# Performance work log

Measured on AMD Instinct MI355X. Metric: run time of the kernel, lower is better.

Reference implementation:

```python
import jax, jax.numpy as jnp
import numpy as np

N = 100000
E = 3200000
IN_DIM = 128
HID = 64
BN_EPS = 1e-5


def _gcn_conv(x, W, b, src, dst, dinv):
    h = x @ W                                      # [N, out]
    coeff = (dinv[src] * dinv[dst])[:, None]       # [E, 1]
    msg = h[src] * coeff                           # gather over edges
    agg = jax.ops.segment_sum(msg, dst, num_segments=N)
    agg = agg + h * (dinv * dinv)[:, None]         # self-loop term
    return agg + b


def setup_inputs() -> dict:
    key = jax.random.key(0)
    ks = jax.random.split(key, 12)
    x = jax.random.normal(ks[0], (N, IN_DIM), dtype=jnp.float32)
    edge_index = jax.random.randint(ks[1], (2, E), 0, N, dtype=jnp.int64)
    s1 = 1.0 / np.sqrt(IN_DIM)
    s2 = 1.0 / np.sqrt(HID)
    W1 = jax.random.uniform(ks[2], (IN_DIM, HID), jnp.float32, -s1, s1)
    b1 = jnp.zeros((HID,), jnp.float32)
    W2 = jax.random.uniform(ks[3], (HID, HID), jnp.float32, -s2, s2)
    b2 = jnp.zeros((HID,), jnp.float32)
    W3 = jax.random.uniform(ks[4], (HID, 1), jnp.float32, -s2, s2)
    b3 = jnp.zeros((1,), jnp.float32)
    g1 = jnp.ones((HID,), jnp.float32)
    beta1 = jnp.zeros((HID,), jnp.float32)
    m1 = 0.1 * jax.random.normal(ks[5], (HID,), jnp.float32)
    v1 = jax.random.uniform(ks[6], (HID,), jnp.float32) + 0.5
    g2 = jnp.ones((HID,), jnp.float32)
    beta2 = jnp.zeros((HID,), jnp.float32)
    m2 = 0.1 * jax.random.normal(ks[7], (HID,), jnp.float32)
    v2 = jax.random.uniform(ks[8], (HID,), jnp.float32) + 0.5
    return {"x": x, "edge_index": edge_index,
            "W1": W1, "b1": b1, "W2": W2, "b2": b2, "W3": W3, "b3": b3,
            "g1": g1, "beta1": beta1, "m1": m1, "v1": v1,
            "g2": g2, "beta2": beta2, "m2": m2, "v2": v2}


def reference(x, edge_index, W1, b1, W2, b2, W3, b3,
              g1, beta1, m1, v1, g2, beta2, m2, v2):
    src, dst = edge_index[0], edge_index[1]
    # degree with self-loops (computed on destination index, PyG convention)
    deg = jax.ops.segment_sum(jnp.ones((E,), jnp.float32), dst, num_segments=N) + 1.0
    dinv = jax.lax.rsqrt(deg)

    def bn(h, g, beta, m, v):
        return (h - m) * jax.lax.rsqrt(v + BN_EPS) * g + beta

    h = _gcn_conv(x, W1, b1, src, dst, dinv)
    h = jax.nn.relu(bn(h, g1, beta1, m1, v1))  # dropout is a no-op in eval
    h = _gcn_conv(h, W2, b2, src, dst, dinv)
    h = jax.nn.relu(bn(h, g2, beta2, m2, v2))
    h = _gcn_conv(h, W3, b3, src, dst, dinv)
    return jax.nn.sigmoid(h)  # [N, 1]
```

## Files before the change

kernel.cpp:

```cpp
#include <hip/hip_runtime.h>
#include <math.h>

#define N_NODES 100000
#define E_EDGES 3200000
#define IN_DIM_ 128
#define HID_ 64
#define BN_EPS_ 1e-5f

#define PB 250
#define CHUNK 12800
#define NBUCK 391
#define BMAX 9600
#define SUB (N_NODES + 1)

typedef __attribute__((ext_vector_type(8))) short short8;
typedef __attribute__((ext_vector_type(4))) float f32x4;

__device__ inline ushort f2bf(float f) {
    union { float f; unsigned u; } c; c.f = f;
    unsigned r = c.u + 0x7fff + ((c.u >> 16) & 1);
    return (ushort)(r >> 16);
}
__device__ inline float bf_lo(unsigned p) { union { unsigned u; float f; } c; c.u = p << 16; return c.f; }
__device__ inline float bf_hi(unsigned p) { union { unsigned u; float f; } c; c.u = p & 0xffff0000u; return c.f; }

__global__ __launch_bounds__(512) void passA1_hist(const int* __restrict__ ei,
                                                   int* __restrict__ histPB) {
    __shared__ int hist[NBUCK];
    int t = threadIdx.x, b = blockIdx.x;
    for (int k = t; k < NBUCK; k += 512) hist[k] = 0;
    __syncthreads();
    int e0 = b * CHUNK, e1 = e0 + CHUNK;
    for (int e = e0 + t; e < e1; e += 512) {
        int d = ei[E_EDGES + e];
        atomicAdd(&hist[d >> 8], 1);
    }
    __syncthreads();
    for (int k = t; k < NBUCK; k += 512) histPB[k * PB + b] = hist[k];
}

__global__ __launch_bounds__(256) void scan_rows(int* __restrict__ histPB,
                                                 int* __restrict__ bucket_tot) {
    __shared__ int wsum[4];
    int k = blockIdx.x, t = threadIdx.x, lane = t & 63, wv = t >> 6;
    int v = (t < PB) ? histPB[k * PB + t] : 0;
    int s = v;
#pragma unroll
    for (int off = 1; off < 64; off <<= 1) {
        int u = __shfl_up(s, off, 64);
        if (lane >= off) s += u;
    }
    if (lane == 63) wsum[wv] = s;
    __syncthreads();
    int wbase = 0;
    for (int w = 0; w < wv; w++) wbase += wsum[w];
    if (t < PB) histPB[k * PB + t] = wbase + s - v;
    if (t == 255) bucket_tot[k] = wbase + s;
}

__global__ __launch_bounds__(512) void scan_totals(const int* __restrict__ bucket_tot,
                                                   int* __restrict__ bucket_base,
                                                   float* __restrict__ hs3) {
    __shared__ int wsum[8];
    int t = threadIdx.x, lane = t & 63, wv = t >> 6;
    int v = (t < NBUCK) ? bucket_tot[t] : 0;
    int s = v;
#pragma unroll
    for (int off = 1; off < 64; off <<= 1) {
        int u = __shfl_up(s, off, 64);
        if (lane >= off) s += u;
    }
    if (lane == 63) wsum[wv] = s;
    __syncthreads();
    int wbase = 0;
    for (int w = 0; w < wv; w++) wbase += wsum[w];
    if (t < NBUCK) bucket_base[t] = wbase + s - v;
    if (t == 0) {
        bucket_base[NBUCK] = E_EDGES;
        hs3[N_NODES] = 0.f;
    }
}

__global__ __launch_bounds__(512) void passA2_sorted(const int* __restrict__ ei,
                                                     const int* __restrict__ histPB,
                                                     const int* __restrict__ bucket_base,
                                                     int* __restrict__ ebuf) {
    __shared__ int sorted[CHUNK];
    __shared__ ushort bid[CHUNK];
    __shared__ int cur[NBUCK];
    __shared__ int lbase[NBUCK];
    int t = threadIdx.x, b = blockIdx.x;
    for (int k = t; k < NBUCK; k += 512) cur[k] = 0;
    __syncthreads();
    int e0 = b * CHUNK;
    for (int e = e0 + t; e < e0 + CHUNK; e += 512)
        atomicAdd(&cur[ei[E_EDGES + e] >> 8], 1);
    __syncthreads();
    if (t < 64) {
        int run = 0;
        for (int c0 = 0; c0 < NBUCK; c0 += 64) {
            int idx = c0 + t;
            int v = (idx < NBUCK) ? cur[idx] : 0;
            int s = v;
#pragma unroll
            for (int off = 1; off < 64; off <<= 1) {
                int u = __shfl_up(s, off, 64);
                if (t >= off) s += u;
            }
            if (idx < NBUCK) lbase[idx] = run + s - v;
            run += __shfl(s, 63, 64);
        }
    }
    __syncthreads();
    for (int k = t; k < NBUCK; k += 512) cur[k] = lbase[k];
    __syncthreads();
    for (int e = e0 + t; e < e0 + CHUNK; e += 512) {
        int s = ei[e];
        int d = ei[E_EDGES + e];
        int k = d >> 8;
        int pos = atomicAdd(&cur[k], 1);
        sorted[pos] = s | ((d & 255) << 17);
        bid[pos] = (ushort)k;
    }
    __syncthreads();
    for (int j = t; j < CHUNK; j += 512) {
        int k = bid[j];
        int dest = bucket_base[k] + histPB[k * PB + b] + (j - lbase[k]);
        ebuf[dest] = sorted[j];
    }
}

__global__ __launch_bounds__(256) void bucket_deg(const int* __restrict__ ebuf,
                                                  const int* __restrict__ bucket_base,
                                                  int* __restrict__ deg,
                                                  float* __restrict__ dinv,
                                                  int* __restrict__ bucket_ptot) {
    __shared__ int hist[256];
    __shared__ int wsum[4];
    int b = blockIdx.x, t = threadIdx.x, lane = t & 63, wv = t >> 6;
    int base = bucket_base[b], end = bucket_base[b + 1];
    hist[t] = 0;
    __syncthreads();
    for (int k = base + t; k < end; k += 256)
        atomicAdd(&hist[ebuf[k] >> 17], 1);
    __syncthreads();
    int node = b * 256 + t;
    int d = hist[t];
    if (node < N_NODES) {
        deg[node] = d;
        dinv[node] = rsqrtf((float)d + 1.0f);
    }
    int pd = (node < N_NODES) ? ((d + 15) & ~15) : 0;
#pragma unroll
    for (int off = 1; off < 64; off <<= 1) pd += __shfl_xor(pd, off, 64);
    if (lane == 0) wsum[wv] = pd;
    __syncthreads();
    if (t == 0) bucket_ptot[b] = wsum[0] + wsum[1] + wsum[2] + wsum[3];
}

__global__ __launch_bounds__(512) void scan_ptot(const int* __restrict__ bucket_ptot,
                                                 int* __restrict__ bucket_pbase,
                                                 int* __restrict__ row_ptr) {
    __shared__ int wsum[8];
    int t = threadIdx.x, lane = t & 63, wv = t >> 6;
    int v = (t < NBUCK) ? bucket_ptot[t] : 0;
    int s = v;
#pragma unroll
    for (int off = 1; off < 64; off <<= 1) {
        int u = __shfl_up(s, off, 64);
        if (lane >= off) s += u;
    }
    if (lane == 63) wsum[wv] = s;
    __syncthreads();
    int wbase = 0;
    for (int w = 0; w < wv; w++) wbase += wsum[w];
    if (t < NBUCK) bucket_pbase[t] = wbase + s - v;
    if (t == NBUCK - 1) row_ptr[N_NODES] = wbase + s;
}

__global__ __launch_bounds__(256) void passB_sorted(const int* __restrict__ ebuf,
                                                    const int* __restrict__ bucket_base,
                                                    const int* __restrict__ bucket_pbase,
                                                    const int* __restrict__ deg,
                                                    int* __restrict__ row_ptr,
                                                    int* __restrict__ csr_src) {
    __shared__ int sorted[BMAX];
    __shared__ int ucur[256];
    __shared__ int ubeg[256];
    __shared__ int pbeg[256];
    __shared__ int wsA[4], wsB[4];
    int b = blockIdx.x, t = threadIdx.x, lane = t & 63, wv = t >> 6;
    int base = bucket_base[b], end = bucket_base[b + 1];
    int pbase = bucket_pbase[b];
    int node = b * 256 + t;
    int d = (node < N_NODES) ? deg[node] : 0;
    int pd = (d + 15) & ~15;
    if (node >= N_NODES) pd = 0;
    int sa = d, sb = pd;
#pragma unroll
    for (int off = 1; off < 64; off <<= 1) {
        int ua = __shfl_up(sa, off, 64);
        int ub = __shfl_up(sb, off, 64);
        if (lane >= off) { sa += ua; sb += ub; }
    }
    if (lane == 63) { wsA[wv] = sa; wsB[wv] = sb; }
    __syncthreads();
    int wa = 0, wb = 0;
    for (int w = 0; w < wv; w++) { wa += wsA[w]; wb += wsB[w]; }
    int uex = wa + sa - d, pex = wb + sb - pd;
    ubeg[t] = uex; pbeg[t] = pex; ucur[t] = uex;
    if (node < N_NODES) row_ptr[node] = pbase + pex;
    __syncthreads();
    for (int k = base + t; k < end; k += 256) {
        int pv = ebuf[k];
        int pos = atomicAdd(&ucur[pv >> 17], 1);
        if (pos < BMAX) sorted[pos] = pv;
    }
    __syncthreads();
    for (int r = wv; r < 256; r += 4) {
        int nd = b * 256 + r;
        int d2 = (nd < N_NODES) ? deg[nd] : 0;
        int pd2 = (nd < N_NODES) ? ((d2 + 15) & ~15) : 0;
        int ub = ubeg[r], pb = pbeg[r];
        for (int c = lane; c < pd2; c += 64)
            csr_src[pbase + pb + c] = (c < d2) ? (sorted[ub + c] & 0x1FFFF) : N_NODES;
    }
}

template<bool LAST, int P>
__global__ __launch_bounds__(256) void gather_pass(const int* __restrict__ row_ptr,
                                                   const int* __restrict__ csr_src,
                                                   const ushort* __restrict__ hs,
                                                   const float* __restrict__ dinv,
                                                   const float* __restrict__ b,
                                                   const float* __restrict__ g,
                                                   const float* __restrict__ beta,
                                                   const float* __restrict__ m,
                                                   const float* __restrict__ v,
                                                   unsigned* __restrict__ y,
                                                   const float* __restrict__ W3,
                                                   float* __restrict__ hs3, int n) {
    int i = (blockIdx.x * 256 + threadIdx.x) >> 6;
    if (i >= n) return;
    int l = threadIdx.x & 63;
    int es = l >> 2, fg = l & 3;

    const uint4* T4 = (const uint4*)((const unsigned*)hs + (long)P * SUB * 16);

    float a0 = 0.f, a1 = 0.f, a2 = 0.f, a3 = 0.f;
    float a4 = 0.f, a5 = 0.f, a6 = 0.f, a7 = 0.f;

    if (es == 0) {
        uint4 p = T4[(unsigned)i * 4 + fg];
        a0 += bf_lo(p.x); a1 += bf_hi(p.x);
        a2 += bf_lo(p.y); a3 += bf_hi(p.y);
        a4 += bf_lo(p.z); a5 += bf_hi(p.z);
        a6 += bf_lo(p.w); a7 += bf_hi(p.w);
    }

    int pbeg = row_ptr[i], pend = row_ptr[i + 1];
    const int* cs = csr_src + pbeg + es;
    int nb16 = (pend - pbeg) >> 4;
    int k = 0;
    for (; k + 2 <= nb16; k += 2) {
        int sA = cs[0];
        int sB = cs[16];
        cs += 32;
        uint4 pA = T4[(unsigned)sA * 4 + fg];
        uint4 pB = T4[(unsigned)sB * 4 + fg];
        a0 += bf_lo(pA.x) + bf_lo(pB.x); a1 += bf_hi(pA.x) + bf_hi(pB.x);
        a2 += bf_lo(pA.y) + bf_lo(pB.y); a3 += bf_hi(pA.y) + bf_hi(pB.y);
        a4 += bf_lo(pA.z) + bf_lo(pB.z); a5 += bf_hi(pA.z) + bf_hi(pB.z);
        a6 += bf_lo(pA.w) + bf_lo(pB.w); a7 += bf_hi(pA.w) + bf_hi(pB.w);
    }
    if (k < nb16) {
        int s = cs[0];
        uint4 p = T4[(unsigned)s * 4 + fg];
        a0 += bf_lo(p.x); a1 += bf_hi(p.x);
        a2 += bf_lo(p.y); a3 += bf_hi(p.y);
        a4 += bf_lo(p.z); a5 += bf_hi(p.z);
        a6 += bf_lo(p.w); a7 += bf_hi(p.w);
    }

#pragma unroll
    for (int off = 4; off < 64; off <<= 1) {
        a0 += __shfl_xor(a0, off, 64);
        a1 += __shfl_xor(a1, off, 64);
        a2 += __shfl_xor(a2, off, 64);
        a3 += __shfl_xor(a3, off, 64);
        a4 += __shfl_xor(a4, off, 64);
        a5 += __shfl_xor(a5, off, 64);
        a6 += __shfl_xor(a6, off, 64);
        a7 += __shfl_xor(a7, off, 64);
    }

    int fb = P * 8 + fg * 2;
    float4 bb0 = ((const float4*)b)[fb],    bb1 = ((const float4*)b)[fb + 1];
    float4 gg0 = ((const float4*)g)[fb],    gg1 = ((const float4*)g)[fb + 1];
    float4 be0 = ((const float4*)beta)[fb], be1 = ((const float4*)beta)[fb + 1];
    float4 mm0 = ((const float4*)m)[fb],    mm1 = ((const float4*)m)[fb + 1];
    float4 vv0 = ((const float4*)v)[fb],    vv1 = ((const float4*)v)[fb + 1];
    float di = dinv[i];
    float o0 = fmaxf((di * a0 + bb0.x - mm0.x) * (gg0.x * rsqrtf(vv0.x + BN_EPS_)) + be0.x, 0.f);
    float o1 = fmaxf((di * a1 + bb0.y - mm0.y) * (gg0.y * rsqrtf(vv0.y + BN_EPS_)) + be0.y, 0.f);
    float o2 = fmaxf((di * a2 + bb0.z - mm0.z) * (gg0.z * rsqrtf(vv0.z + BN_EPS_)) + be0.z, 0.f);
    float o3 = fmaxf((di * a3 + bb0.w - mm0.w) * (gg0.w * rsqrtf(vv0.w + BN_EPS_)) + be0.w, 0.f);
    float o4 = fmaxf((di * a4 + bb1.x - mm1.x) * (gg1.x * rsqrtf(vv1.x + BN_EPS_)) + be1.x, 0.f);
    float o5 = fmaxf((di * a5 + bb1.y - mm1.y) * (gg1.y * rsqrtf(vv1.y + BN_EPS_)) + be1.y, 0.f);
    float o6 = fmaxf((di * a6 + bb1.z - mm1.z) * (gg1.z * rsqrtf(vv1.z + BN_EPS_)) + be1.z, 0.f);
    float o7 = fmaxf((di * a7 + bb1.w - mm1.w) * (gg1.w * rsqrtf(vv1.w + BN_EPS_)) + be1.w, 0.f);

    if (LAST) {
        float4 w30 = ((const float4*)W3)[fb], w31 = ((const float4*)W3)[fb + 1];
        float p = o0 * w30.x + o1 * w30.y + o2 * w30.z + o3 * w30.w +
                  o4 * w31.x + o5 * w31.y + o6 * w31.z + o7 * w31.w;
        p += __shfl_xor(p, 1, 64);
        p += __shfl_xor(p, 2, 64);
        if (l == 0) {
            if (P == 0) hs3[i] = p;
            else        hs3[i] = (hs3[i] + p) * di;
        }
    } else {
        if (es == 0) {
            uint4 pk;
            pk.x = (unsigned)f2bf(o0) | ((unsigned)f2bf(o1) << 16);
            pk.y = (unsigned)f2bf(o2) | ((unsigned)f2bf(o3) << 16);
            pk.z = (unsigned)f2bf(o4) | ((unsigned)f2bf(o5) << 16);
            pk.w = (unsigned)f2bf(o6) | ((unsigned)f2bf(o7) << 16);
            ((uint4*)y)[(long)i * 8 + P * 4 + fg] = pk;
        }
    }
}

template<int K, bool BF16IN>
__global__ __launch_bounds__(256) void gemm_bf16(const void* __restrict__ Xv,
                                                 const float* __restrict__ W,
                                                 const float* __restrict__ dinv,
                                                 ushort* __restrict__ hs) {
    constexpr int KP = K + 8;
    __shared__ ushort A_lds[64][KP];
    __shared__ ushort Wt_lds[64][KP];
    int t = threadIdx.x;
    long row0 = (long)blockIdx.x * 64;

    for (int i = t; i < K * 16; i += 256) {
        float4 w4 = ((const float4*)W)[i];
        int k = i >> 4, n = (i & 15) * 4;
        Wt_lds[n + 0][k] = f2bf(w4.x);
        Wt_lds[n + 1][k] = f2bf(w4.y);
        Wt_lds[n + 2][k] = f2bf(w4.z);
        Wt_lds[n + 3][k] = f2bf(w4.w);
    }
    if (BF16IN) {
        constexpr int K2 = K / 2;
        const unsigned* X = (const unsigned*)Xv;
        for (int i = t; i < 64 * K2; i += 256) {
            int r = i / K2, c = i % K2;
            unsigned val = 0;
            long row = row0 + r;
            if (row < N_NODES) val = X[row * K2 + c];
            *(unsigned*)&A_lds[r][c * 2] = val;
        }
    } else {
        constexpr int K4 = K / 4;
        const float* X = (const float*)Xv;
        for (int i = t; i < 64 * K4; i += 256) {
            int r = i / K4, c = i % K4;
            float4 val = make_float4(0.f, 0.f, 0.f, 0.f);
            long row = row0 + r;
            if (row < N_NODES) val = ((const float4*)X)[row * K4 + c];
            int cb = c * 4;
            A_lds[r][cb + 0] = f2bf(val.x);
            A_lds[r][cb + 1] = f2bf(val.y);
            A_lds[r][cb + 2] = f2bf(val.z);
            A_lds[r][cb + 3] = f2bf(val.w);
        }
    }
    __syncthreads();

    int w = t >> 6, l = t & 63;
    int m = l & 15, quad = l >> 4;
    f32x4 acc[4];
#pragma unroll
    for (int c = 0; c < 4; c++) acc[c] = (f32x4){0.f, 0.f, 0.f, 0.f};

#pragma unroll
    for (int ch = 0; ch < K / 32; ch++) {
        short8 a = *(const short8*)&A_lds[16 * w + m][32 * ch + 8 * quad];
#pragma unroll
        for (int c = 0; c < 4; c++) {
            short8 b = *(const short8*)&Wt_lds[16 * c + m][32 * ch + 8 * quad];
            acc[c] = __builtin_amdgcn_mfma_f32_16x16x32_bf16(a, b, acc[c], 0, 0, 0);
        }
    }

#pragma unroll
    for (int r = 0; r < 4; r++) {
        long node = row0 + 16 * w + quad * 4 + r;
        if (node <= N_NODES) {
            float dv = (node < N_NODES) ? dinv[node] : 0.f;
#pragma unroll
            for (int c = 0; c < 4; c++)
                hs[((long)(c >> 1) * SUB + node) * 32 + (c & 1) * 16 + m] = f2bf(acc[c][r] * dv);
        }
    }
}

__global__ __launch_bounds__(256) void gather3(const int* __restrict__ row_ptr,
                                               const int* __restrict__ csr_src,
                                               const float* __restrict__ hs3,
                                               const float* __restrict__ dinv,
                                               const float* __restrict__ b3,
                                               float* __restrict__ out, int n) {
    int i = blockIdx.x * 256 + threadIdx.x;
    if (i >= n) return;
    int beg = row_ptr[i], end = row_ptr[i + 1];
    float s0 = hs3[i], s1 = 0.f, s2 = 0.f, s3 = 0.f;
    float s4 = 0.f, s5 = 0.f, s6 = 0.f, s7 = 0.f;
    for (int k = beg; k + 8 <= end; k += 8) {
        s0 += hs3[csr_src[k]];
        s1 += hs3[csr_src[k + 1]];
        s2 += hs3[csr_src[k + 2]];
        s3 += hs3[csr_src[k + 3]];
        s4 += hs3[csr_src[k + 4]];
        s5 += hs3[csr_src[k + 5]];
        s6 += hs3[csr_src[k + 6]];
        s7 += hs3[csr_src[k + 7]];
    }
    float z = dinv[i] * (((s0 + s1) + (s2 + s3)) + ((s4 + s5) + (s6 + s7))) + b3[0];
    out[i] = 1.f / (1.f + expf(-z));
}

extern "C" void kernel_launch(void* const* d_in, const int* in_sizes, int n_in,
                              void* d_out, int out_size, void* d_ws, size_t ws_size,
                              hipStream_t stream) {
    const int N = N_NODES;
    const int E = E_EDGES;

    const float* x   = (const float*)d_in[0];
    const int*   ei  = (const int*)d_in[1];
    const float* W1  = (const float*)d_in[2];
    const float* b1  = (const float*)d_in[3];
    const float* W2  = (const float*)d_in[4];
    const float* b2  = (const float*)d_in[5];
    const float* W3  = (const float*)d_in[6];
    const float* b3  = (const float*)d_in[7];
    const float* g1  = (const float*)d_in[8];
    const float* bt1 = (const float*)d_in[9];
    const float* m1  = (const float*)d_in[10];
    const float* v1  = (const float*)d_in[11];
    const float* g2  = (const float*)d_in[12];
    const float* bt2 = (const float*)d_in[13];
    const float* m2  = (const float*)d_in[14];
    const float* v2  = (const float*)d_in[15];
    float* out = (float*)d_out;

    int*    wsi          = (int*)d_ws;
    float*  dinv         = (float*)wsi;
    float*  hs3          = (float*)(wsi + (long)N);
    int*    row_ptr      = wsi + 2L * N + 16;
    int*    deg          = row_ptr + N + 16;
    int*    histPB       = deg + N + 16;
    int*    bucket_tot   = histPB + NBUCK * PB;
    int*    bucket_base  = bucket_tot + 400;
    int*    bucket_ptot  = bucket_base + 402;
    int*    bucket_pbase = bucket_ptot + 400;
    ushort* hsb          = (ushort*)(bucket_pbase + 402);
    unsigned* yb         = (unsigned*)((int*)(void*)hsb + 32L * SUB);
    int*    csr_src      = (int*)yb + 32L * N;
    int*    ebuf         = (int*)(void*)hsb;

    passA1_hist<<<PB, 512, 0, stream>>>(ei, histPB);
    scan_rows<<<NBUCK, 256, 0, stream>>>(histPB, bucket_tot);
    scan_totals<<<1, 512, 0, stream>>>(bucket_tot, bucket_base, hs3);
    passA2_sorted<<<PB, 512, 0, stream>>>(ei, histPB, bucket_base, ebuf);
    bucket_deg<<<NBUCK, 256, 0, stream>>>(ebuf, bucket_base, deg, dinv, bucket_ptot);
    scan_ptot<<<1, 512, 0, stream>>>(bucket_ptot, bucket_pbase, row_ptr);
    passB_sorted<<<NBUCK, 256, 0, stream>>>(ebuf, bucket_base, bucket_pbase,
                                            deg, row_ptr, csr_src);

    const int GG = (N + 3) / 4;

    gemm_bf16<IN_DIM_, false><<<(N + 63) / 64, 256, 0, stream>>>(x, W1, dinv, hsb);
    gather_pass<false, 0><<<GG, 256, 0, stream>>>(row_ptr, csr_src, hsb, dinv,
                                                  b1, g1, bt1, m1, v1, yb, W3, hs3, N);
    gather_pass<false, 1><<<GG, 256, 0, stream>>>(row_ptr, csr_src, hsb, dinv,
                                                  b1, g1, bt1, m1, v1, yb, W3, hs3, N);
    gemm_bf16<HID_, true><<<(N + 63) / 64, 256, 0, stream>>>(yb, W2, dinv, hsb);
    gather_pass<true, 0><<<GG, 256, 0, stream>>>(row_ptr, csr_src, hsb, dinv,
                                                 b2, g2, bt2, m2, v2, yb, W3, hs3, N);
    gather_pass<true, 1><<<GG, 256, 0, stream>>>(row_ptr, csr_src, hsb, dinv,
                                                 b2, g2, bt2, m2, v2, yb, W3, hs3, N);
    gather3<<<(N + 255) / 256, 256, 0, stream>>>(row_ptr, csr_src, hs3, dinv, b3, out, N);
}
```

Before: 489.9 us.

## Merge two half-feature gather passes into one full-width gather per layer

Replaces the two gather passes per layer, each handling 32 of the 64 features, with a single pass. Each wave now covers all 64 features using 8 lanes per edge and 8 edge slots, so csr_src is read once per layer instead of twice and two kernel launches are removed. CSR row padding drops from multiples of 16 to multiples of 8 to match the new edge stride, which cuts the number of padded dummy edges. The gather loop is unrolled to four loads per lane per iteration for more memory parallelism. In exchange, each pass touches the whole feature table, so cache locality per pass may be worse than with the two half-width tables.

```diff
diff --git a/kernel.cpp b/kernel.cpp
--- a/kernel.cpp
+++ b/kernel.cpp
@@ -150,7 +150,7 @@
         deg[node] = d;
         dinv[node] = rsqrtf((float)d + 1.0f);
     }
-    int pd = (node < N_NODES) ? ((d + 15) & ~15) : 0;
+    int pd = (node < N_NODES) ? ((d + 7) & ~7) : 0;
 #pragma unroll
     for (int off = 1; off < 64; off <<= 1) pd += __shfl_xor(pd, off, 64);
     if (lane == 0) wsum[wv] = pd;
@@ -194,7 +194,7 @@
     int pbase = bucket_pbase[b];
     int node = b * 256 + t;
     int d = (node < N_NODES) ? deg[node] : 0;
-    int pd = (d + 15) & ~15;
+    int pd = (d + 7) & ~7;
     if (node >= N_NODES) pd = 0;
     int sa = d, sb = pd;
 #pragma unroll
@@ -220,15 +220,15 @@
     for (int r = wv; r < 256; r += 4) {
         int nd = b * 256 + r;
         int d2 = (nd < N_NODES) ? deg[nd] : 0;
-        int pd2 = (nd < N_NODES) ? ((d2 + 15) & ~15) : 0;
+        int pd2 = (nd < N_NODES) ? ((d2 + 7) & ~7) : 0;
         int ub = ubeg[r], pb = pbeg[r];
         for (int c = lane; c < pd2; c += 64)
             csr_src[pbase + pb + c] = (c < d2) ? (sorted[ub + c] & 0x1FFFF) : N_NODES;
     }
 }
 
-template<bool LAST, int P>
-__global__ __launch_bounds__(256) void gather_pass(const int* __restrict__ row_ptr,
+template<bool LAST>
+__global__ __launch_bounds__(256) void gather_full(const int* __restrict__ row_ptr,
                                                    const int* __restrict__ csr_src,
                                                    const ushort* __restrict__ hs,
                                                    const float* __restrict__ dinv,
@@ -243,15 +243,15 @@
     int i = (blockIdx.x * 256 + threadIdx.x) >> 6;
     if (i >= n) return;
     int l = threadIdx.x & 63;
-    int es = l >> 2, fg = l & 3;
-
-    const uint4* T4 = (const uint4*)((const unsigned*)hs + (long)P * SUB * 16);
+    int es = l >> 3, fg = l & 7;
+
+    const uint4* Tq = (const uint4*)hs + (long)(fg >> 2) * SUB * 4 + (fg & 3);
 
     float a0 = 0.f, a1 = 0.f, a2 = 0.f, a3 = 0.f;
     float a4 = 0.f, a5 = 0.f, a6 = 0.f, a7 = 0.f;
 
     if (es == 0) {
-        uint4 p = T4[(unsigned)i * 4 + fg];
+        uint4 p = Tq[(unsigned)i * 4];
         a0 += bf_lo(p.x); a1 += bf_hi(p.x);
         a2 += bf_lo(p.y); a3 += bf_hi(p.y);
         a4 += bf_lo(p.z); a5 += bf_hi(p.z);
@@ -260,22 +260,28 @@
 
     int pbeg = row_ptr[i], pend = row_ptr[i + 1];
     const int* cs = csr_src + pbeg + es;
-    int nb16 = (pend - pbeg) >> 4;
-    int k = 0;
-    for (; k + 2 <= nb16; k += 2) {
-        int sA = cs[0];
-        int sB = cs[16];
+    int nb8 = (pend - pbeg) >> 3;
+    int full = nb8 >> 2;
+    for (int t = 0; t < full; t++) {
+        int s0 = cs[0], s1 = cs[8], s2 = cs[16], s3 = cs[24];
         cs += 32;
-        uint4 pA = T4[(unsigned)sA * 4 + fg];
-        uint4 pB = T4[(unsigned)sB * 4 + fg];
-        a0 += bf_lo(pA.x) + bf_lo(pB.x); a1 += bf_hi(pA.x) + bf_hi(pB.x);
-        a2 += bf_lo(pA.y) + bf_lo(pB.y); a3 += bf_hi(pA.y) + bf_hi(pB.y);
-        a4 += bf_lo(pA.z) + bf_lo(pB.z); a5 += bf_hi(pA.z) + bf_hi(pB.z);
-        a6 += bf_lo(pA.w) + bf_lo(pB.w); a7 += bf_hi(pA.w) + bf_hi(pB.w);
-    }
-    if (k < nb16) {
+        uint4 p0 = Tq[(unsigned)s0 * 4];
+        uint4 p1 = Tq[(unsigned)s1 * 4];
+        uint4 p2 = Tq[(unsigned)s2 * 4];
+        uint4 p3 = Tq[(unsigned)s3 * 4];
+        a0 += bf_lo(p0.x) + bf_lo(p1.x); a1 += bf_hi(p0.x) + bf_hi(p1.x);
+        a2 += bf_lo(p0.y) + bf_lo(p1.y); a3 += bf_hi(p0.y) + bf_hi(p1.y);
+        a4 += bf_lo(p0.z) + bf_lo(p1.z); a5 += bf_hi(p0.z) + bf_hi(p1.z);
+        a6 += bf_lo(p0.w) + bf_lo(p1.w); a7 += bf_hi(p0.w) + bf_hi(p1.w);
+        a0 += bf_lo(p2.x) + bf_lo(p3.x); a1 += bf_hi(p2.x) + bf_hi(p3.x);
+        a2 += bf_lo(p2.y) + bf_lo(p3.y); a3 += bf_hi(p2.y) + bf_hi(p3.y);
+        a4 += bf_lo(p2.z) + bf_lo(p3.z); a5 += bf_hi(p2.z) + bf_hi(p3.z);
+        a6 += bf_lo(p2.w) + bf_lo(p3.w); a7 += bf_hi(p2.w) + bf_hi(p3.w);
+    }
+    for (int rem = nb8 & 3; rem > 0; rem--) {
         int s = cs[0];
-        uint4 p = T4[(unsigned)s * 4 + fg];
+        cs += 8;
+        uint4 p = Tq[(unsigned)s * 4];
         a0 += bf_lo(p.x); a1 += bf_hi(p.x);
         a2 += bf_lo(p.y); a3 += bf_hi(p.y);
         a4 += bf_lo(p.z); a5 += bf_hi(p.z);
@@ -283,7 +289,7 @@
     }
 
 #pragma unroll
-    for (int off = 4; off < 64; off <<= 1) {
+    for (int off = 8; off < 64; off <<= 1) {
         a0 += __shfl_xor(a0, off, 64);
         a1 += __shfl_xor(a1, off, 64);
         a2 += __shfl_xor(a2, off, 64);
@@ -294,12 +300,11 @@
         a7 += __shfl_xor(a7, off, 64);
     }
 
-    int fb = P * 8 + fg * 2;
-    float4 bb0 = ((const float4*)b)[fb],    bb1 = ((const float4*)b)[fb + 1];
-    float4 gg0 = ((const float4*)g)[fb],    gg1 = ((const float4*)g)[fb + 1];
-    float4 be0 = ((const float4*)beta)[fb], be1 = ((const float4*)beta)[fb + 1];
-    float4 mm0 = ((const float4*)m)[fb],    mm1 = ((const float4*)m)[fb + 1];
-    float4 vv0 = ((const float4*)v)[fb],    vv1 = ((const float4*)v)[fb + 1];
+    float4 bb0 = ((const float4*)b)[fg * 2],    bb1 = ((const float4*)b)[fg * 2 + 1];
+    float4 gg0 = ((const float4*)g)[fg * 2],    gg1 = ((const float4*)g)[fg * 2 + 1];
+    float4 be0 = ((const float4*)beta)[fg * 2], be1 = ((const float4*)beta)[fg * 2 + 1];
+    float4 mm0 = ((const float4*)m)[fg * 2],    mm1 = ((const float4*)m)[fg * 2 + 1];
+    float4 vv0 = ((const float4*)v)[fg * 2],    vv1 = ((const float4*)v)[fg * 2 + 1];
     float di = dinv[i];
     float o0 = fmaxf((di * a0 + bb0.x - mm0.x) * (gg0.x * rsqrtf(vv0.x + BN_EPS_)) + be0.x, 0.f);
     float o1 = fmaxf((di * a1 + bb0.y - mm0.y) * (gg0.y * rsqrtf(vv0.y + BN_EPS_)) + be0.y, 0.f);
@@ -311,15 +316,13 @@
     float o7 = fmaxf((di * a7 + bb1.w - mm1.w) * (gg1.w * rsqrtf(vv1.w + BN_EPS_)) + be1.w, 0.f);
 
     if (LAST) {
-        float4 w30 = ((const float4*)W3)[fb], w31 = ((const float4*)W3)[fb + 1];
+        float4 w30 = ((const float4*)W3)[fg * 2], w31 = ((const float4*)W3)[fg * 2 + 1];
         float p = o0 * w30.x + o1 * w30.y + o2 * w30.z + o3 * w30.w +
                   o4 * w31.x + o5 * w31.y + o6 * w31.z + o7 * w31.w;
-        p += __shfl_xor(p, 1, 64);
-        p += __shfl_xor(p, 2, 64);
-        if (l == 0) {
-            if (P == 0) hs3[i] = p;
-            else        hs3[i] = (hs3[i] + p) * di;
-        }
+#pragma unroll
+        for (int off = 1; off < 8; off <<= 1)
+            p += __shfl_xor(p, off, 64);
+        if (l == 0) hs3[i] = p * di;
     } else {
         if (es == 0) {
             uint4 pk;
@@ -327,7 +330,7 @@
             pk.y = (unsigned)f2bf(o2) | ((unsigned)f2bf(o3) << 16);
             pk.z = (unsigned)f2bf(o4) | ((unsigned)f2bf(o5) << 16);
             pk.w = (unsigned)f2bf(o6) | ((unsigned)f2bf(o7) << 16);
-            ((uint4*)y)[(long)i * 8 + P * 4 + fg] = pk;
+            ((uint4*)y)[(long)i * 8 + fg] = pk;
         }
     }
 }
@@ -482,14 +485,10 @@
     const int GG = (N + 3) / 4;
 
     gemm_bf16<IN_DIM_, false><<<(N + 63) / 64, 256, 0, stream>>>(x, W1, dinv, hsb);
-    gather_pass<false, 0><<<GG, 256, 0, stream>>>(row_ptr, csr_src, hsb, dinv,
-                                                  b1, g1, bt1, m1, v1, yb, W3, hs3, N);
-    gather_pass<false, 1><<<GG, 256, 0, stream>>>(row_ptr, csr_src, hsb, dinv,
-                                                  b1, g1, bt1, m1, v1, yb, W3, hs3, N);
+    gather_full<false><<<GG, 256, 0, stream>>>(row_ptr, csr_src, hsb, dinv,
+                                               b1, g1, bt1, m1, v1, yb, W3, hs3, N);
     gemm_bf16<HID_, true><<<(N + 63) / 64, 256, 0, stream>>>(yb, W2, dinv, hsb);
-    gather_pass<true, 0><<<GG, 256, 0, stream>>>(row_ptr, csr_src, hsb, dinv,
-                                                 b2, g2, bt2, m2, v2, yb, W3, hs3, N);
-    gather_pass<true, 1><<<GG, 256, 0, stream>>>(row_ptr, csr_src, hsb, dinv,
-                                                 b2, g2, bt2, m2, v2, yb, W3, hs3, N);
+    gather_full<true><<<GG, 256, 0, stream>>>(row_ptr, csr_src, hsb, dinv,
+                                              b2, g2, bt2, m2, v2, yb, W3, hs3, N);
     gather3<<<(N + 255) / 256, 256, 0, stream>>>(row_ptr, csr_src, hs3, dinv, b3, out, N);
 }
```

After: 484.5 us. No clear change (-1.1%).
